# Kernel tuning notes

Measured on AMD Instinct MI355X. Metric: run time of the kernel, lower is better.

The kernel has to match this reference:

```python
import jax, jax.numpy as jnp
import numpy as np

INSTANCE_LOSS_WEIGHT = 5.0


def setup_inputs() -> dict:
    key = jax.random.key(0)
    k1, k2 = jax.random.split(key)
    B, NP, NT, H, W = 8, 8, 16, 512, 512
    pred_masks = jax.random.normal(k1, (B, NP, H, W), dtype=jnp.float32)   # logits
    target_masks = jax.random.uniform(k2, (B, NT, H, W), dtype=jnp.float32)  # targets in [0,1]
    return {"pred_masks": pred_masks, "target_masks": target_masks}


def reference(pred_masks, target_masks):
    # Multi-instance branch of SAMLossMultiInstance.forward (pred_masks.shape[1] > 1).
    # Original: per (i,j) pair, mean BCE-with-logits over pixels; pairs where
    # target j is all-zero are skipped (loss_matrix entry stays 0). Then
    # min over targets, mean over preds, mean over batch, * instance_loss_weight.
    #
    # Closed form: BCE(x, t) = softplus(x) - x*t, so
    #   mean_pix BCE(x_i, t_j) = mean(softplus(x_i)) - (x_i . t_j) / HW
    B, NP, H, W = pred_masks.shape
    HW = H * W
    s = jnp.mean(jax.nn.softplus(pred_masks), axis=(-2, -1))               # [B, NP]
    dots = jnp.einsum('bihw,bjhw->bij', pred_masks, target_masks) / HW     # [B, NP, NT]
    loss_matrix = s[:, :, None] - dots                                     # [B, NP, NT]
    # Empty targets are skipped in the original loop -> entry stays 0.
    t_empty = jnp.sum(target_masks, axis=(-2, -1)) == 0                    # [B, NT]
    loss_matrix = jnp.where(t_empty[:, None, :], 0.0, loss_matrix)
    min_losses = jnp.min(loss_matrix, axis=-1)                             # [B, NP]
    instance_loss = jnp.mean(min_losses)
    total_loss = INSTANCE_LOSS_WEIGHT * instance_loss
    return total_loss
```

## Files before the change

kernel.cpp:

```cpp
#include <hip/hip_runtime.h>

#define NB 8
#define NP 8
#define NT 16
#define HW (512 * 512)
#define HW4 (HW / 4)
#define NACC (NP + NP * NT + NT)
#define BLOCKS_PER_B 64
#define THREADS 256
#define ITERS 4

__device__ __forceinline__ float wred(float v) {
#pragma unroll
  for (int off = 32; off > 0; off >>= 1) v += __shfl_down(v, off);
  return v;
}

__device__ __forceinline__ float softplus1(float x) {
  return fmaxf(x, 0.0f) + __logf(1.0f + __expf(-fabsf(x)));
}

__device__ __forceinline__ float sp4(float4 p) {
  return (softplus1(p.x) + softplus1(p.y)) + (softplus1(p.z) + softplus1(p.w));
}

__global__ __launch_bounds__(THREADS, 2) void sam_partial(
    const float* __restrict__ pred, const float* __restrict__ targ,
    float* __restrict__ ws) {
  const int b   = blockIdx.x / BLOCKS_PER_B;
  const int blk = blockIdx.x % BLOCKS_PER_B;
  const int tid = threadIdx.x;

  float sp[NP];
  float ts[NT];
  float dot[NP][NT];
#pragma unroll
  for (int i = 0; i < NP; ++i) sp[i] = 0.0f;
#pragma unroll
  for (int j = 0; j < NT; ++j) ts[j] = 0.0f;
#pragma unroll
  for (int i = 0; i < NP; ++i)
#pragma unroll
    for (int j = 0; j < NT; ++j) dot[i][j] = 0.0f;

  const float4* __restrict__ pb =
      reinterpret_cast<const float4*>(pred) + (size_t)b * NP * HW4;
  const float4* __restrict__ tb =
      reinterpret_cast<const float4*>(targ) + (size_t)b * NT * HW4;

#pragma unroll 1
  for (int it = 0; it < ITERS; ++it) {
    const int idx = blk * (THREADS * ITERS) + it * THREADS + tid;
    float4 p[NP];
#pragma unroll
    for (int i = 0; i < NP; ++i) p[i] = pb[(size_t)i * HW4 + idx];
#pragma unroll
    for (int i = 0; i < NP; ++i) sp[i] += sp4(p[i]);
#pragma unroll
    for (int j = 0; j < NT; ++j) {
      float4 t = tb[(size_t)j * HW4 + idx];
      ts[j] += (t.x + t.y) + (t.z + t.w);
#pragma unroll
      for (int i = 0; i < NP; ++i) {
        dot[i][j] = fmaf(p[i].x, t.x,
                    fmaf(p[i].y, t.y,
                    fmaf(p[i].z, t.z,
                    fmaf(p[i].w, t.w, dot[i][j]))));
      }
    }
  }

  __shared__ float red[4][NACC];
  const int lane = tid & 63;
  const int wid  = tid >> 6;

#pragma unroll
  for (int i = 0; i < NP; ++i) {
    float v = wred(sp[i]);
    if (lane == 0) red[wid][i] = v;
  }
#pragma unroll
  for (int i = 0; i < NP; ++i) {
#pragma unroll
    for (int j = 0; j < NT; ++j) {
      float v = wred(dot[i][j]);
      if (lane == 0) red[wid][NP + i * NT + j] = v;
    }
  }
#pragma unroll
  for (int j = 0; j < NT; ++j) {
    float v = wred(ts[j]);
    if (lane == 0) red[wid][NP + NP * NT + j] = v;
  }
  __syncthreads();
  if (tid < NACC) {
    float v = (red[0][tid] + red[1][tid]) + (red[2][tid] + red[3][tid]);
    atomicAdd(ws + (size_t)b * NACC + tid, v);
  }
}

__global__ void sam_final(const float* __restrict__ ws,
                          float* __restrict__ out) {
  const int t = threadIdx.x;
  const int b = t >> 3;
  const int i = t & 7;
  const float* w = ws + (size_t)b * NACC;
  const float spsum = w[i];
  float m = 3.4e38f;
#pragma unroll
  for (int j = 0; j < NT; ++j) {
    const float tsj = w[NP + NP * NT + j];
    const float v =
        (tsj == 0.0f) ? 0.0f : (spsum - w[NP + i * NT + j]) * (1.0f / HW);
    m = fminf(m, v);
  }
  const float s = wred(m);
  if (t == 0) out[0] = 5.0f * s * (1.0f / 64.0f);
}

extern "C" void kernel_launch(void* const* d_in, const int* in_sizes, int n_in,
                              void* d_out, int out_size, void* d_ws,
                              size_t ws_size, hipStream_t stream) {
  const float* pred = (const float*)d_in[0];
  const float* targ = (const float*)d_in[1];
  float* out = (float*)d_out;
  float* ws = (float*)d_ws;

  hipMemsetAsync(ws, 0, (size_t)NB * NACC * sizeof(float), stream);
  sam_partial<<<dim3(NB * BLOCKS_PER_B), THREADS, 0, stream>>>(pred, targ, ws);
  sam_final<<<1, 64, 0, stream>>>(ws, out);
}
```

Before: 73.17 us.

## Use one float4 per thread and partial shuffle reduction staged in LDS

Each thread now loads a single float4 column from every pred and target channel instead of looping over four. The grid grows to 256 blocks per batch and the occupancy hint rises to 4 blocks per SM. The full 6-step wavefront reduction is replaced by a 3-step shuffle over 8-lane groups, with 32 partial rows written to padded shared memory and summed by 152 threads. This cuts shuffle work per thread and exposes more memory parallelism, but the grid now issues four times as many global atomics and shared-memory writes.

Result: slower. 87.36 us (+19.4%).

```diff
diff --git a/kernel.cpp b/kernel.cpp
--- a/kernel.cpp
+++ b/kernel.cpp
@@ -6,95 +6,76 @@
 #define HW (512 * 512)
 #define HW4 (HW / 4)
 #define NACC (NP + NP * NT + NT)
-#define BLOCKS_PER_B 64
 #define THREADS 256
-#define ITERS 4
-
-__device__ __forceinline__ float wred(float v) {
-#pragma unroll
-  for (int off = 32; off > 0; off >>= 1) v += __shfl_down(v, off);
-  return v;
-}
+#define BLOCKS_PER_B 256
+#define NROW 32
+#define LDSPITCH 153
 
 __device__ __forceinline__ float softplus1(float x) {
   return fmaxf(x, 0.0f) + __logf(1.0f + __expf(-fabsf(x)));
 }
 
-__device__ __forceinline__ float sp4(float4 p) {
-  return (softplus1(p.x) + softplus1(p.y)) + (softplus1(p.z) + softplus1(p.w));
-}
-
-__global__ __launch_bounds__(THREADS, 2) void sam_partial(
+__global__ __launch_bounds__(THREADS, 4) void sam_partial(
     const float* __restrict__ pred, const float* __restrict__ targ,
     float* __restrict__ ws) {
-  const int b   = blockIdx.x / BLOCKS_PER_B;
-  const int blk = blockIdx.x % BLOCKS_PER_B;
+  const int b   = blockIdx.x >> 8;
+  const int blk = blockIdx.x & 255;
   const int tid = threadIdx.x;
+  const int idx = (blk << 8) | tid;
+  const int lane = tid & 63;
+  const int wid  = tid >> 6;
+  const int row  = (wid << 3) | (lane >> 3);
+  const bool wr  = (lane & 7) == 0;
 
-  float sp[NP];
-  float ts[NT];
-  float dot[NP][NT];
-#pragma unroll
-  for (int i = 0; i < NP; ++i) sp[i] = 0.0f;
-#pragma unroll
-  for (int j = 0; j < NT; ++j) ts[j] = 0.0f;
-#pragma unroll
-  for (int i = 0; i < NP; ++i)
-#pragma unroll
-    for (int j = 0; j < NT; ++j) dot[i][j] = 0.0f;
+  __shared__ float red[NROW][LDSPITCH];
 
   const float4* __restrict__ pb =
       reinterpret_cast<const float4*>(pred) + (size_t)b * NP * HW4;
   const float4* __restrict__ tb =
       reinterpret_cast<const float4*>(targ) + (size_t)b * NT * HW4;
 
-#pragma unroll 1
-  for (int it = 0; it < ITERS; ++it) {
-    const int idx = blk * (THREADS * ITERS) + it * THREADS + tid;
-    float4 p[NP];
+  float4 p[NP];
 #pragma unroll
-    for (int i = 0; i < NP; ++i) p[i] = pb[(size_t)i * HW4 + idx];
+  for (int i = 0; i < NP; ++i) p[i] = pb[(size_t)i * HW4 + idx];
+  float4 t[NT];
 #pragma unroll
-    for (int i = 0; i < NP; ++i) sp[i] += sp4(p[i]);
-#pragma unroll
-    for (int j = 0; j < NT; ++j) {
-      float4 t = tb[(size_t)j * HW4 + idx];
-      ts[j] += (t.x + t.y) + (t.z + t.w);
-#pragma unroll
-      for (int i = 0; i < NP; ++i) {
-        dot[i][j] = fmaf(p[i].x, t.x,
-                    fmaf(p[i].y, t.y,
-                    fmaf(p[i].z, t.z,
-                    fmaf(p[i].w, t.w, dot[i][j]))));
-      }
-    }
+  for (int j = 0; j < NT; ++j) t[j] = tb[(size_t)j * HW4 + idx];
+
+#define STASH(a, expr)                                   \
+  {                                                      \
+    float v_ = (expr);                                   \
+    v_ += __shfl_down(v_, 4);                            \
+    v_ += __shfl_down(v_, 2);                            \
+    v_ += __shfl_down(v_, 1);                            \
+    if (wr) red[row][(a)] = v_;                          \
   }
-
-  __shared__ float red[4][NACC];
-  const int lane = tid & 63;
-  const int wid  = tid >> 6;
 
 #pragma unroll
   for (int i = 0; i < NP; ++i) {
-    float v = wred(sp[i]);
-    if (lane == 0) red[wid][i] = v;
+    STASH(i, (softplus1(p[i].x) + softplus1(p[i].y)) +
+             (softplus1(p[i].z) + softplus1(p[i].w)));
   }
 #pragma unroll
   for (int i = 0; i < NP; ++i) {
 #pragma unroll
     for (int j = 0; j < NT; ++j) {
-      float v = wred(dot[i][j]);
-      if (lane == 0) red[wid][NP + i * NT + j] = v;
+      STASH(NP + i * NT + j,
+            fmaf(p[i].x, t[j].x,
+            fmaf(p[i].y, t[j].y,
+            fmaf(p[i].z, t[j].z, p[i].w * t[j].w))));
     }
   }
 #pragma unroll
   for (int j = 0; j < NT; ++j) {
-    float v = wred(ts[j]);
-    if (lane == 0) red[wid][NP + NP * NT + j] = v;
+    STASH(NP + NP * NT + j, (t[j].x + t[j].y) + (t[j].z + t[j].w));
   }
+#undef STASH
+
   __syncthreads();
   if (tid < NACC) {
-    float v = (red[0][tid] + red[1][tid]) + (red[2][tid] + red[3][tid]);
+    float v = 0.0f;
+#pragma unroll
+    for (int r = 0; r < NROW; ++r) v += red[r][tid];
     atomicAdd(ws + (size_t)b * NACC + tid, v);
   }
 }
@@ -114,7 +95,9 @@
         (tsj == 0.0f) ? 0.0f : (spsum - w[NP + i * NT + j]) * (1.0f / HW);
     m = fminf(m, v);
   }
-  const float s = wred(m);
+  float s = m;
+#pragma unroll
+  for (int off = 32; off > 0; off >>= 1) s += __shfl_down(s, off);
   if (t == 0) out[0] = 5.0f * s * (1.0f / 64.0f);
 }
 
```
